# Kernel tuning notes

Measured on AMD Instinct MI355X. Metric: run time of the kernel, lower is better.

## Reference

```python
import jax, jax.numpy as jnp
import numpy as np

# dims
B, L, C = 2, 2048, 256          # batch, seq_len (== max_length), input_dim
H, D = 8, 32                     # num_head, head_dim
W = 3                            # avg-pool window along key axis


def setup_inputs() -> dict:
    key = jax.random.key(0)
    ks = jax.random.split(key, 7)
    g_qk = (2.0 / (C + H * D)) ** 0.5   # GlorotNormal std
    g_v = (2.0 / (C + H)) ** 0.5
    g_pe = (2.0 / (L + C)) ** 0.5
    return {
        "x":  jax.random.normal(ks[0], (B, L, C), dtype=jnp.float32),
        "Wq": jax.random.normal(ks[1], (C, H * D), dtype=jnp.float32) * g_qk,
        "bq": jnp.zeros((H, 1, 1, D), dtype=jnp.float32),
        "Wk": jax.random.normal(ks[2], (C, H * D), dtype=jnp.float32) * g_qk,
        "bk": jnp.zeros((H, 1, 1, D), dtype=jnp.float32),
        "Wv": jax.random.normal(ks[3], (C, H), dtype=jnp.float32) * g_v,
        "pe": jax.random.normal(ks[4], (L, C), dtype=jnp.float32) * g_pe,
    }


def reference(x, Wq, bq, Wk, bk, Wv, pe):
    b, l, _ = x.shape
    xq = x + pe                                   # (B,L,C) -- pe added to q and k inputs only
    q = (xq @ Wq).reshape(b, l, H, D).transpose(2, 0, 1, 3) + bq   # (H,B,L,D)
    k = (xq @ Wk).reshape(b, l, H, D).transpose(2, 0, 1, 3) + bk   # (H,B,L,D)
    v = (x @ Wv).transpose(2, 0, 1)               # (H,B,L) scalar gate per (head, pos)

    attn = jnp.einsum('hbqd,hbkd->hbqk', q, k) * (float(D) ** -0.5)  # (H,B,Lq,Lk)
    attn = jax.nn.softmax(attn, axis=-1)
    # band_part(-1, 0): keep lower triangle (q >= k), applied AFTER softmax
    causal = jnp.tril(jnp.ones((l, l), dtype=bool))
    attn = jnp.where(causal, attn, jnp.zeros((), attn.dtype))
    # scalar value gate along the query axis
    attn = attn * v[..., None]                    # (H,B,Lq,Lk)
    # avg-pool window W along key axis, SAME padding, pads excluded from count (TF semantics)
    sums = jax.lax.reduce_window(attn, 0.0, jax.lax.add, (1, 1, 1, W), (1, 1, 1, 1), 'SAME')
    counts = jax.lax.reduce_window(jnp.ones((l,), attn.dtype), 0.0, jax.lax.add, (W,), (1,), 'SAME')
    attn = sums / counts                          # broadcast (Lk,) over (H,B,Lq,Lk)
    # permute to (B,Lq,Lk,H) then global_mode sum over Lq  ->  (B,Lk,H)
    return jnp.sum(attn, axis=2).transpose(1, 2, 0)
```

## Files before the change

### kernel.cpp

```cpp
#include <hip/hip_runtime.h>

#define B 2
#define L 2048
#define C 256
#define H 8
#define D 32
#define HB 16
#define SCALE 0.17677669529663687f
#define LOG2E 1.4426950408889634f
#define QS (SCALE * LOG2E)

using bf16x8 = __attribute__((ext_vector_type(8))) __bf16;
using f32x4  = __attribute__((ext_vector_type(4))) float;

static __device__ inline unsigned short f2bf(float f) {
    unsigned u = __float_as_uint(f);
    return (unsigned short)((u + 0x7fffu + ((u >> 16) & 1u)) >> 16);
}
static __device__ inline unsigned pk2(float lo, float hi) {
    return (unsigned)f2bf(lo) | ((unsigned)f2bf(hi) << 16);
}

static __device__ inline float fexp2(float x) {
#if __has_builtin(__builtin_amdgcn_exp2f)
    return __builtin_amdgcn_exp2f(x);
#else
    float r; asm("v_exp_f32 %0, %1" : "=v"(r) : "v"(x)); return r;
#endif
}

__global__ __launch_bounds__(256) void prep_kernel(
    const float* __restrict__ x,
    const float* __restrict__ Wq,
    const float* __restrict__ Wk,
    const float* __restrict__ Wv,
    unsigned short* __restrict__ WqT,
    unsigned short* __restrict__ WkT,
    float* __restrict__ Vo)
{
    __shared__ float smem[64 * 65];
    const int t = threadIdx.x;

    if (blockIdx.x < 512) {
        float (*xrT)[8] = (float(*)[8])smem;
        float* vred = smem + 256 * 8;
        const int row0 = blockIdx.x * 8;
        const int b = row0 >> 11;
#pragma unroll
        for (int i = 0; i < 8; ++i)
            xrT[t][i] = x[(row0 + i) * C + t];
        __syncthreads();
        {
            const int cc = t >> 6, sub = t & 63, vi = sub >> 3, vh = sub & 7;
            float va = 0.f;
            for (int c = cc * 64; c < cc * 64 + 64; ++c)
                va += xrT[c][vi] * Wv[c * H + vh];
            vred[(cc * 8 + vi) * 8 + vh] = va;
        }
        __syncthreads();
        if (t < 64) {
            const int i2 = t >> 3, h2 = t & 7;
            const float v = vred[(0 * 8 + i2) * 8 + h2] + vred[(1 * 8 + i2) * 8 + h2] +
                            vred[(2 * 8 + i2) * 8 + h2] + vred[(3 * 8 + i2) * 8 + h2];
            const int l = (row0 + i2) & (L - 1);
            Vo[(h2 * B + b) * L + l] = v;
        }
    } else {
        const int bb = blockIdx.x - 512;
        const int mat = bb >> 4;
        const int tile = bb & 15, ci = tile >> 2, ni = tile & 3;
        const float* W = mat ? Wk : Wq;
        unsigned short* WT = mat ? WkT : WqT;
        const float s = mat ? 1.0f : QS;
        const int c0 = ci * 64, n0 = ni * 64;
        float (*ld)[65] = (float(*)[65])smem;
        const int tr = t >> 4, tc = (t & 15) * 4;
#pragma unroll
        for (int p = 0; p < 4; ++p) {
            const int lc = p * 16 + tr;
            const float4 v = *(const float4*)&W[(c0 + lc) * (H * D) + n0 + tc];
            ld[lc][tc] = v.x; ld[lc][tc + 1] = v.y;
            ld[lc][tc + 2] = v.z; ld[lc][tc + 3] = v.w;
        }
        __syncthreads();
#pragma unroll
        for (int p = 0; p < 4; ++p) {
            const int nl = p * 16 + tr;
            const unsigned lo = pk2(ld[tc][nl] * s, ld[tc + 1][nl] * s);
            const unsigned hi = pk2(ld[tc + 2][nl] * s, ld[tc + 3][nl] * s);
            uint2 u; u.x = lo; u.y = hi;
            *(uint2*)&WT[(n0 + nl) * C + c0 + tc] = u;
        }
    }
}

__global__ __launch_bounds__(256) void qk_gemm_kernel(
    const float* __restrict__ x, const float* __restrict__ pe,
    const unsigned short* __restrict__ WqT, const unsigned short* __restrict__ WkT,
    const float* __restrict__ bq, const float* __restrict__ bk,
    unsigned short* __restrict__ Qo, unsigned short* __restrict__ Ko)
{
    __shared__ uint4 xqs[16][32];
    const int t = threadIdx.x;
    const int w = t >> 6, lane = t & 63;
    const int quad = lane >> 4, col = lane & 15;
    const int row0 = (blockIdx.x >> 2) * 16;
    const int n0 = (blockIdx.x & 3) * 64;

    {
        const int srow = t >> 4, sc = (t & 15) * 16;
        const int grow = row0 + srow;
        const int gl = grow & (L - 1);
        const float* xp = x + (size_t)grow * C + sc;
        const float* pp = pe + (size_t)gl * C + sc;
        const float4 a0 = ((const float4*)xp)[0], a1 = ((const float4*)xp)[1];
        const float4 a2 = ((const float4*)xp)[2], a3 = ((const float4*)xp)[3];
        const float4 p0 = ((const float4*)pp)[0], p1 = ((const float4*)pp)[1];
        const float4 p2 = ((const float4*)pp)[2], p3 = ((const float4*)pp)[3];
        uint4 u0, u1;
        u0.x = pk2(a0.x + p0.x, a0.y + p0.y);
        u0.y = pk2(a0.z + p0.z, a0.w + p0.w);
        u0.z = pk2(a1.x + p1.x, a1.y + p1.y);
        u0.w = pk2(a1.z + p1.z, a1.w + p1.w);
        u1.x = pk2(a2.x + p2.x, a2.y + p2.y);
        u1.y = pk2(a2.z + p2.z, a2.w + p2.w);
        u1.z = pk2(a3.x + p3.x, a3.y + p3.y);
        u1.w = pk2(a3.z + p3.z, a3.w + p3.w);
        const int cb = (t & 15) * 2;
        xqs[srow][(cb + 0) ^ (srow & 7)] = u0;
        xqs[srow][(cb + 1) ^ (srow & 7)] = u1;
    }
    __syncthreads();

    bf16x8 af[8];
#pragma unroll
    for (int kk = 0; kk < 8; ++kk)
        af[kk] = *(const bf16x8*)&xqs[col][(kk * 4 + quad) ^ (col & 7)];

    const int n = n0 + w * 16 + col;
    const unsigned short* wq = WqT + (size_t)n * C;
    const unsigned short* wk = WkT + (size_t)n * C;
    f32x4 accq = {0.f, 0.f, 0.f, 0.f};
    f32x4 acck = {0.f, 0.f, 0.f, 0.f};
#pragma unroll
    for (int kk = 0; kk < 8; ++kk) {
        const bf16x8 bq8 = *(const bf16x8*)(wq + kk * 32 + quad * 8);
        const bf16x8 bk8 = *(const bf16x8*)(wk + kk * 32 + quad * 8);
        accq = __builtin_amdgcn_mfma_f32_16x16x32_bf16(af[kk], bq8, accq, 0, 0, 0);
        acck = __builtin_amdgcn_mfma_f32_16x16x32_bf16(af[kk], bk8, acck, 0, 0, 0);
    }

    const int h = n >> 5, d = n & 31;
    const float bqv = bq[n] * QS;
    const float bkv = bk[n];
#pragma unroll
    for (int r = 0; r < 4; ++r) {
        const int m = quad * 4 + r;
        const int grow = row0 + m, b = grow >> 11, l = grow & (L - 1);
        const size_t o = ((size_t)(h * B + b) * L + l) * D + d;
        Qo[o] = f2bf(accq[r] + bqv);
        Ko[o] = f2bf(acck[r] + bkv);
    }
}

__global__ __launch_bounds__(256) void passA_kernel(
    const __bf16* __restrict__ Qb, const __bf16* __restrict__ Kb,
    const float* __restrict__ V, float* __restrict__ G)
{
    __shared__ float lredA[4][4][4][16];
    __shared__ float lredB[4][4][4][16];
    const int tid = threadIdx.x;
    const int w = tid >> 6, lane = tid & 63;
    const int quad = lane >> 4, col = lane & 15;
    const int xcd = blockIdx.x & 7, g = blockIdx.x >> 3;
    const int hb = xcd * 2 + (g >> 6), p = g & 63;
    const __bf16* Qp = Qb + (size_t)hb * L * D;
    const __bf16* Kp = Kb + (size_t)hb * L * D;

    const bf16x8 qfa = *(const bf16x8*)(Qp + ((2 * p) * 16 + col) * D + quad * 8);
    const bf16x8 qfb = *(const bf16x8*)(Qp + ((2 * p + 1) * 16 + col) * D + quad * 8);
    const f32x4 zero = {0.f, 0.f, 0.f, 0.f};

    float la0 = 0.f, la1 = 0.f, la2 = 0.f, la3 = 0.f;
    float lb0 = 0.f, lb1 = 0.f, lb2 = 0.f, lb3 = 0.f;
    const __bf16* kp = Kp + (w * 512 + col) * D + quad * 8;
#pragma unroll 4
    for (int kt = 0; kt < 32; ++kt) {
        const bf16x8 kf = *(const bf16x8*)kp;
        kp += 16 * D;
        f32x4 a = __builtin_amdgcn_mfma_f32_16x16x32_bf16(qfa, kf, zero, 0, 0, 0);
        f32x4 bb = __builtin_amdgcn_mfma_f32_16x16x32_bf16(qfb, kf, zero, 0, 0, 0);
        la0 += fexp2(a[0]);  lb0 += fexp2(bb[0]);
        la1 += fexp2(a[1]);  lb1 += fexp2(bb[1]);
        la2 += fexp2(a[2]);  lb2 += fexp2(bb[2]);
        la3 += fexp2(a[3]);  lb3 += fexp2(bb[3]);
    }
    lredA[w][quad][0][col] = la0;  lredB[w][quad][0][col] = lb0;
    lredA[w][quad][1][col] = la1;  lredB[w][quad][1][col] = lb1;
    lredA[w][quad][2][col] = la2;  lredB[w][quad][2][col] = lb2;
    lredA[w][quad][3][col] = la3;  lredB[w][quad][3][col] = lb3;
    __syncthreads();
    if (tid < 32) {
        const int r8 = tid & 15;
        const int qd = r8 >> 2, r = r8 & 3;
        const float* base = (tid < 16) ? &lredA[0][0][0][0] : &lredB[0][0][0][0];
        float s = 0.f;
#pragma unroll
        for (int w2 = 0; w2 < 4; ++w2) {
            const float* pp = base + ((w2 * 4 + qd) * 4 + r) * 16;
#pragma unroll
            for (int c2 = 0; c2 < 16; ++c2) s += pp[c2];
        }
        const int qt = 2 * p + (tid >> 4);
        const int qq = hb * L + qt * 16 + r8;
        G[qq] = V[qq] / s;
    }
}

__global__ __launch_bounds__(256) void passB_kernel(
    const __bf16* __restrict__ Qb, const __bf16* __restrict__ Kb,
    const float* __restrict__ G, float* __restrict__ S)
{
    __shared__ float sred[2][4][4][16];
    const int tid = threadIdx.x;
    const int w = tid >> 6, lane = tid & 63;
    const int quad = lane >> 4, col = lane & 15;
    const int xcd = blockIdx.x & 7, g = blockIdx.x >> 3;
    const int hb = xcd * 2 + (g >> 6), p = g & 63;
    const int kb0 = 2 * p, kb1 = 2 * p + 1;
    const __bf16* Qp = Qb + (size_t)hb * L * D;
    const __bf16* Kp = Kb + (size_t)hb * L * D;
    const float* Gp = G + hb * L;

    const bf16x8 kf0 = *(const bf16x8*)(Kp + (kb0 * 16 + col) * D + quad * 8);
    const bf16x8 kf1 = *(const bf16x8*)(Kp + (kb1 * 16 + col) * D + quad * 8);
    const f32x4 zero = {0.f, 0.f, 0.f, 0.f};
    const int kidx0 = kb0 * 16 + col;
    const int kidx1 = kb1 * 16 + col;

    float s0 = 0.f, s1 = 0.f;
    int qt = kb0 + w;
    if (qt < 128) {
        const bf16x8 qf = *(const bf16x8*)(Qp + (qt * 16 + col) * D + quad * 8);
        const float4 gg = *(const float4*)(Gp + qt * 16 + quad * 4);
        const int qbase = qt * 16 + quad * 4;
        f32x4 a0 = __builtin_amdgcn_mfma_f32_16x16x32_bf16(qf, kf0, zero, 0, 0, 0);
        if (w == 0) {
            s0 += (qbase + 0 >= kidx0) ? fexp2(a0[0]) * gg.x : 0.f;
            s0 += (qbase + 1 >= kidx0) ? fexp2(a0[1]) * gg.y : 0.f;
            s0 += (qbase + 2 >= kidx0) ? fexp2(a0[2]) * gg.z : 0.f;
            s0 += (qbase + 3 >= kidx0) ? fexp2(a0[3]) * gg.w : 0.f;
        } else {
            s0 += fexp2(a0[0]) * gg.x + fexp2(a0[1]) * gg.y +
                  fexp2(a0[2]) * gg.z + fexp2(a0[3]) * gg.w;
            f32x4 a1 = __builtin_amdgcn_mfma_f32_16x16x32_bf16(qf, kf1, zero, 0, 0, 0);
            if (w == 1) {
                s1 += (qbase + 0 >= kidx1) ? fexp2(a1[0]) * gg.x : 0.f;
                s1 += (qbase + 1 >= kidx1) ? fexp2(a1[1]) * gg.y : 0.f;
                s1 += (qbase + 2 >= kidx1) ? fexp2(a1[2]) * gg.z : 0.f;
                s1 += (qbase + 3 >= kidx1) ? fexp2(a1[3]) * gg.w : 0.f;
            } else {
                s1 += fexp2(a1[0]) * gg.x + fexp2(a1[1]) * gg.y +
                      fexp2(a1[2]) * gg.z + fexp2(a1[3]) * gg.w;
            }
        }
        qt += 4;
    }
    for (; qt < 128; qt += 4) {
        const bf16x8 qf = *(const bf16x8*)(Qp + (qt * 16 + col) * D + quad * 8);
        const float4 gg = *(const float4*)(Gp + qt * 16 + quad * 4);
        f32x4 a0 = __builtin_amdgcn_mfma_f32_16x16x32_bf16(qf, kf0, zero, 0, 0, 0);
        f32x4 a1 = __builtin_amdgcn_mfma_f32_16x16x32_bf16(qf, kf1, zero, 0, 0, 0);
        s0 += fexp2(a0[0]) * gg.x + fexp2(a0[1]) * gg.y +
              fexp2(a0[2]) * gg.z + fexp2(a0[3]) * gg.w;
        s1 += fexp2(a1[0]) * gg.x + fexp2(a1[1]) * gg.y +
              fexp2(a1[2]) * gg.z + fexp2(a1[3]) * gg.w;
    }
    sred[0][w][quad][col] = s0;
    sred[1][w][quad][col] = s1;
    __syncthreads();
    if (tid < 32) {
        const int c = tid & 15, which = tid >> 4;
        float s = 0.f;
#pragma unroll
        for (int j = 0; j < 16; ++j) s += sred[which][j >> 2][j & 3][c];
        S[hb * L + (2 * p + which) * 16 + c] = s;
    }
}

__global__ __launch_bounds__(256) void pool_kernel(
    const float* __restrict__ S, float* __restrict__ out)
{
    const int flat = blockIdx.x * 256 + threadIdx.x;
    const int h = flat & 7;
    const int k = (flat >> 3) & (L - 1);
    const int b = flat >> 14;
    const float* Sb = S + (h * B + b) * L;
    float s = Sb[k];
    float cnt = 1.f;
    if (k > 0)     { s += Sb[k - 1]; cnt += 1.f; }
    if (k < L - 1) { s += Sb[k + 1]; cnt += 1.f; }
    out[flat] = s / cnt;
}

extern "C" void kernel_launch(void* const* d_in, const int* in_sizes, int n_in,
                              void* d_out, int out_size, void* d_ws, size_t ws_size,
                              hipStream_t stream)
{
    const float* x  = (const float*)d_in[0];
    const float* Wq = (const float*)d_in[1];
    const float* bq = (const float*)d_in[2];
    const float* Wk = (const float*)d_in[3];
    const float* bk = (const float*)d_in[4];
    const float* Wv = (const float*)d_in[5];
    const float* pe = (const float*)d_in[6];
    float* out = (float*)d_out;

    unsigned short* Qbf = (unsigned short*)d_ws;
    unsigned short* Kbf = Qbf + (size_t)HB * L * D;
    float* Vo = (float*)(Kbf + (size_t)HB * L * D);
    float* G  = Vo + (size_t)HB * L;
    float* S  = G  + (size_t)HB * L;
    unsigned short* WqT = (unsigned short*)(S + (size_t)HB * L);
    unsigned short* WkT = WqT + (size_t)C * H * D;

    prep_kernel<<<544, 256, 0, stream>>>(x, Wq, Wk, Wv, WqT, WkT, Vo);
    qk_gemm_kernel<<<1024, 256, 0, stream>>>(x, pe, WqT, WkT, bq, bk, Qbf, Kbf);
    passA_kernel<<<1024, 256, 0, stream>>>(
        (const __bf16*)Qbf, (const __bf16*)Kbf, Vo, G);
    passB_kernel<<<1024, 256, 0, stream>>>(
        (const __bf16*)Qbf, (const __bf16*)Kbf, G, S);
    pool_kernel<<<(B * L * H) / 256, 256, 0, stream>>>(S, out);
}
```

Before: 107.2 us.

## Fuse V projection into QK GEMM, pool into passB, pre-swizzle weights

Splits the prep kernel: weight transposition now writes weights directly in MFMA fragment order so GEMM B-loads become contiguous, while the x@Wv projection is folded into the QK GEMM blocks of quarter 0. The pool kernel is removed and replaced by a last-block-done atomic counter in passB that performs the window average per head-batch. Cross-lane reductions in passA/passB switch from shared-memory sums to wave shuffles, and launch bounds add occupancy hints. This saves kernel launches and memory traffic, but adds atomic/fence overhead and puts extra work on a quarter of the GEMM blocks.

```diff
diff --git a/kernel.cpp b/kernel.cpp
--- a/kernel.cpp
+++ b/kernel.cpp
@@ -29,86 +29,57 @@
 #endif
 }
 
-__global__ __launch_bounds__(256) void prep_kernel(
-    const float* __restrict__ x,
+__global__ __launch_bounds__(256) void wtrans_kernel(
     const float* __restrict__ Wq,
     const float* __restrict__ Wk,
-    const float* __restrict__ Wv,
     unsigned short* __restrict__ WqT,
     unsigned short* __restrict__ WkT,
-    float* __restrict__ Vo)
-{
-    __shared__ float smem[64 * 65];
+    unsigned int* __restrict__ cnt)
+{
     const int t = threadIdx.x;
-
-    if (blockIdx.x < 512) {
-        float (*xrT)[8] = (float(*)[8])smem;
-        float* vred = smem + 256 * 8;
-        const int row0 = blockIdx.x * 8;
-        const int b = row0 >> 11;
-#pragma unroll
-        for (int i = 0; i < 8; ++i)
-            xrT[t][i] = x[(row0 + i) * C + t];
-        __syncthreads();
-        {
-            const int cc = t >> 6, sub = t & 63, vi = sub >> 3, vh = sub & 7;
-            float va = 0.f;
-            for (int c = cc * 64; c < cc * 64 + 64; ++c)
-                va += xrT[c][vi] * Wv[c * H + vh];
-            vred[(cc * 8 + vi) * 8 + vh] = va;
-        }
-        __syncthreads();
-        if (t < 64) {
-            const int i2 = t >> 3, h2 = t & 7;
-            const float v = vred[(0 * 8 + i2) * 8 + h2] + vred[(1 * 8 + i2) * 8 + h2] +
-                            vred[(2 * 8 + i2) * 8 + h2] + vred[(3 * 8 + i2) * 8 + h2];
-            const int l = (row0 + i2) & (L - 1);
-            Vo[(h2 * B + b) * L + l] = v;
-        }
-    } else {
-        const int bb = blockIdx.x - 512;
-        const int mat = bb >> 4;
-        const int tile = bb & 15, ci = tile >> 2, ni = tile & 3;
-        const float* W = mat ? Wk : Wq;
-        unsigned short* WT = mat ? WkT : WqT;
-        const float s = mat ? 1.0f : QS;
-        const int c0 = ci * 64, n0 = ni * 64;
-        float (*ld)[65] = (float(*)[65])smem;
-        const int tr = t >> 4, tc = (t & 15) * 4;
-#pragma unroll
-        for (int p = 0; p < 4; ++p) {
-            const int lc = p * 16 + tr;
-            const float4 v = *(const float4*)&W[(c0 + lc) * (H * D) + n0 + tc];
-            ld[lc][tc] = v.x; ld[lc][tc + 1] = v.y;
-            ld[lc][tc + 2] = v.z; ld[lc][tc + 3] = v.w;
-        }
-        __syncthreads();
-#pragma unroll
-        for (int p = 0; p < 4; ++p) {
-            const int nl = p * 16 + tr;
-            const unsigned lo = pk2(ld[tc][nl] * s, ld[tc + 1][nl] * s);
-            const unsigned hi = pk2(ld[tc + 2][nl] * s, ld[tc + 3][nl] * s);
-            uint2 u; u.x = lo; u.y = hi;
-            *(uint2*)&WT[(n0 + nl) * C + c0 + tc] = u;
-        }
-    }
-}
-
-__global__ __launch_bounds__(256) void qk_gemm_kernel(
+    if (blockIdx.x == 0 && t < HB) cnt[t] = 0;
+
+    const int mat = blockIdx.x >> 5;
+    const int fid = (blockIdx.x & 31) * 256 + t;
+    const int col = fid & 15;
+    const int quad = (fid >> 4) & 3;
+    const int kk = (fid >> 6) & 7;
+    const int nt = fid >> 9;
+    const int n = nt * 16 + col;
+    const int c0 = kk * 32 + quad * 8;
+    const float* W = mat ? Wk : Wq;
+    unsigned short* WT = mat ? WkT : WqT;
+    const float s = mat ? 1.0f : QS;
+
+    float v[8];
+#pragma unroll
+    for (int j = 0; j < 8; ++j)
+        v[j] = W[(c0 + j) * (H * D) + n] * s;
+    uint4 u;
+    u.x = pk2(v[0], v[1]); u.y = pk2(v[2], v[3]);
+    u.z = pk2(v[4], v[5]); u.w = pk2(v[6], v[7]);
+    *(uint4*)(WT + (size_t)fid * 8) = u;
+}
+
+__global__ __launch_bounds__(256, 4) void qk_gemm_kernel(
     const float* __restrict__ x, const float* __restrict__ pe,
     const unsigned short* __restrict__ WqT, const unsigned short* __restrict__ WkT,
     const float* __restrict__ bq, const float* __restrict__ bk,
-    unsigned short* __restrict__ Qo, unsigned short* __restrict__ Ko)
+    const float* __restrict__ Wv,
+    unsigned short* __restrict__ Qo, unsigned short* __restrict__ Ko,
+    float* __restrict__ Vo)
 {
     __shared__ uint4 xqs[16][32];
+    __shared__ float vpart[16][16][9];
     const int t = threadIdx.x;
     const int w = t >> 6, lane = t & 63;
     const int quad = lane >> 4, col = lane & 15;
     const int row0 = (blockIdx.x >> 2) * 16;
-    const int n0 = (blockIdx.x & 3) * 64;
+    const int quarter = blockIdx.x & 3;
+    const int doV = (quarter == 0);
 
     {
-        const int srow = t >> 4, sc = (t & 15) * 16;
+        const int srow = t >> 4, scIdx = t & 15, sc = scIdx * 16;
         const int grow = row0 + srow;
         const int gl = grow & (L - 1);
         const float* xp = x + (size_t)grow * C + sc;
@@ -126,30 +97,60 @@
         u1.y = pk2(a2.z + p2.z, a2.w + p2.w);
         u1.z = pk2(a3.x + p3.x, a3.y + p3.y);
         u1.w = pk2(a3.z + p3.z, a3.w + p3.w);
-        const int cb = (t & 15) * 2;
+        const int cb = scIdx * 2;
         xqs[srow][(cb + 0) ^ (srow & 7)] = u0;
         xqs[srow][(cb + 1) ^ (srow & 7)] = u1;
-    }
-    __syncthreads();
+
+        if (doV) {
+            float vp[8];
+#pragma unroll
+            for (int hh = 0; hh < 8; ++hh) vp[hh] = 0.f;
+            const float xs[16] = {a0.x, a0.y, a0.z, a0.w, a1.x, a1.y, a1.z, a1.w,
+                                  a2.x, a2.y, a2.z, a2.w, a3.x, a3.y, a3.z, a3.w};
+#pragma unroll
+            for (int j = 0; j < 16; ++j) {
+                const float4 wv0 = *(const float4*)&Wv[(sc + j) * H];
+                const float4 wv1 = *(const float4*)&Wv[(sc + j) * H + 4];
+                vp[0] += xs[j] * wv0.x; vp[1] += xs[j] * wv0.y;
+                vp[2] += xs[j] * wv0.z; vp[3] += xs[j] * wv0.w;
+                vp[4] += xs[j] * wv1.x; vp[5] += xs[j] * wv1.y;
+                vp[6] += xs[j] * wv1.z; vp[7] += xs[j] * wv1.w;
+            }
+#pragma unroll
+            for (int hh = 0; hh < 8; ++hh) vpart[srow][scIdx][hh] = vp[hh];
+        }
+    }
+    __syncthreads();
+
+    if (doV && t < 128) {
+        const int srow2 = t >> 3, h2 = t & 7;
+        float v = 0.f;
+#pragma unroll
+        for (int i = 0; i < 16; ++i) v += vpart[srow2][i][h2];
+        const int grow = row0 + srow2, b = grow >> 11, l = grow & (L - 1);
+        Vo[(h2 * B + b) * L + l] = v;
+    }
 
     bf16x8 af[8];
 #pragma unroll
     for (int kk = 0; kk < 8; ++kk)
         af[kk] = *(const bf16x8*)&xqs[col][(kk * 4 + quad) ^ (col & 7)];
 
-    const int n = n0 + w * 16 + col;
-    const unsigned short* wq = WqT + (size_t)n * C;
-    const unsigned short* wk = WkT + (size_t)n * C;
+    const int nt = quarter * 4 + w;
+    const unsigned short* wq = WqT + ((size_t)nt * 8 * 4 * 16) * 8;
+    const unsigned short* wk = WkT + ((size_t)nt * 8 * 4 * 16) * 8;
+    const int foff = (quad * 16 + col) * 8;
     f32x4 accq = {0.f, 0.f, 0.f, 0.f};
     f32x4 acck = {0.f, 0.f, 0.f, 0.f};
 #pragma unroll
     for (int kk = 0; kk < 8; ++kk) {
-        const bf16x8 bq8 = *(const bf16x8*)(wq + kk * 32 + quad * 8);
-        const bf16x8 bk8 = *(const bf16x8*)(wk + kk * 32 + quad * 8);
+        const bf16x8 bq8 = *(const bf16x8*)(wq + kk * 512 + foff);
+        const bf16x8 bk8 = *(const bf16x8*)(wk + kk * 512 + foff);
         accq = __builtin_amdgcn_mfma_f32_16x16x32_bf16(af[kk], bq8, accq, 0, 0, 0);
         acck = __builtin_amdgcn_mfma_f32_16x16x32_bf16(af[kk], bk8, acck, 0, 0, 0);
     }
 
+    const int n = nt * 16 + col;
     const int h = n >> 5, d = n & 31;
     const float bqv = bq[n] * QS;
     const float bkv = bk[n];
@@ -163,12 +164,11 @@
     }
 }
 
-__global__ __launch_bounds__(256) void passA_kernel(
+__global__ __launch_bounds__(256, 4) void passA_kernel(
     const __bf16* __restrict__ Qb, const __bf16* __restrict__ Kb,
     const float* __restrict__ V, float* __restrict__ G)
 {
-    __shared__ float lredA[4][4][4][16];
-    __shared__ float lredB[4][4][4][16];
+    __shared__ float lred2[4][4][8];
     const int tid = threadIdx.x;
     const int w = tid >> 6, lane = tid & 63;
     const int quad = lane >> 4, col = lane & 15;
@@ -181,8 +181,9 @@
     const bf16x8 qfb = *(const bf16x8*)(Qp + ((2 * p + 1) * 16 + col) * D + quad * 8);
     const f32x4 zero = {0.f, 0.f, 0.f, 0.f};
 
-    float la0 = 0.f, la1 = 0.f, la2 = 0.f, la3 = 0.f;
-    float lb0 = 0.f, lb1 = 0.f, lb2 = 0.f, lb3 = 0.f;
+    float acc[8];
+#pragma unroll
+    for (int i = 0; i < 8; ++i) acc[i] = 0.f;
     const __bf16* kp = Kp + (w * 512 + col) * D + quad * 8;
 #pragma unroll 4
     for (int kt = 0; kt < 32; ++kt) {
@@ -190,38 +191,42 @@
         kp += 16 * D;
         f32x4 a = __builtin_amdgcn_mfma_f32_16x16x32_bf16(qfa, kf, zero, 0, 0, 0);
         f32x4 bb = __builtin_amdgcn_mfma_f32_16x16x32_bf16(qfb, kf, zero, 0, 0, 0);
-        la0 += fexp2(a[0]);  lb0 += fexp2(bb[0]);
-        la1 += fexp2(a[1]);  lb1 += fexp2(bb[1]);
-        la2 += fexp2(a[2]);  lb2 += fexp2(bb[2]);
-        la3 += fexp2(a[3]);  lb3 += fexp2(bb[3]);
-    }
-    lredA[w][quad][0][col] = la0;  lredB[w][quad][0][col] = lb0;
-    lredA[w][quad][1][col] = la1;  lredB[w][quad][1][col] = lb1;
-    lredA[w][quad][2][col] = la2;  lredB[w][quad][2][col] = lb2;
-    lredA[w][quad][3][col] = la3;  lredB[w][quad][3][col] = lb3;
+        acc[0] += fexp2(a[0]);  acc[4] += fexp2(bb[0]);
+        acc[1] += fexp2(a[1]);  acc[5] += fexp2(bb[1]);
+        acc[2] += fexp2(a[2]);  acc[6] += fexp2(bb[2]);
+        acc[3] += fexp2(a[3]);  acc[7] += fexp2(bb[3]);
+    }
+#pragma unroll
+    for (int i = 0; i < 8; ++i) {
+        float v = acc[i];
+        v += __shfl_xor(v, 1);
+        v += __shfl_xor(v, 2);
+        v += __shfl_xor(v, 4);
+        v += __shfl_xor(v, 8);
+        acc[i] = v;
+    }
+    if (col == 0) {
+#pragma unroll
+        for (int i = 0; i < 8; ++i) lred2[w][quad][i] = acc[i];
+    }
     __syncthreads();
     if (tid < 32) {
-        const int r8 = tid & 15;
-        const int qd = r8 >> 2, r = r8 & 3;
-        const float* base = (tid < 16) ? &lredA[0][0][0][0] : &lredB[0][0][0][0];
-        float s = 0.f;
-#pragma unroll
-        for (int w2 = 0; w2 < 4; ++w2) {
-            const float* pp = base + ((w2 * 4 + qd) * 4 + r) * 16;
-#pragma unroll
-            for (int c2 = 0; c2 < 16; ++c2) s += pp[c2];
-        }
-        const int qt = 2 * p + (tid >> 4);
-        const int qq = hb * L + qt * 16 + r8;
+        const int tile = tid >> 4, idx = tid & 15;
+        const int qd = idx >> 2, r = idx & 3;
+        const float s = lred2[0][qd][tile * 4 + r] + lred2[1][qd][tile * 4 + r] +
+                        lred2[2][qd][tile * 4 + r] + lred2[3][qd][tile * 4 + r];
+        const int qq = hb * L + (2 * p + tile) * 16 + idx;
         G[qq] = V[qq] / s;
     }
 }
 
-__global__ __launch_bounds__(256) void passB_kernel(
+__global__ __launch_bounds__(256, 4) void passB_kernel(
     const __bf16* __restrict__ Qb, const __bf16* __restrict__ Kb,
-    const float* __restrict__ G, float* __restrict__ S)
-{
-    __shared__ float sred[2][4][4][16];
+    const float* __restrict__ G, float* __restrict__ S,
+    unsigned int* __restrict__ cnt, float* __restrict__ out)
+{
+    __shared__ float sred[4][2][16];
+    __shared__ int lastf;
     const int tid = threadIdx.x;
     const int w = tid >> 6, lane = tid & 63;
     const int quad = lane >> 4, col = lane & 15;
@@ -266,6 +271,7 @@
         }
         qt += 4;
     }
+#pragma unroll 2
     for (; qt < 128; qt += 4) {
         const bf16x8 qf = *(const bf16x8*)(Qp + (qt * 16 + col) * D + quad * 8);
         const float4 gg = *(const float4*)(Gp + qt * 16 + quad * 4);
@@ -276,31 +282,37 @@
         s1 += fexp2(a1[0]) * gg.x + fexp2(a1[1]) * gg.y +
               fexp2(a1[2]) * gg.z + fexp2(a1[3]) * gg.w;
     }
-    sred[0][w][quad][col] = s0;
-    sred[1][w][quad][col] = s1;
+    s0 += __shfl_xor(s0, 16); s0 += __shfl_xor(s0, 32);
+    s1 += __shfl_xor(s1, 16); s1 += __shfl_xor(s1, 32);
+    if (lane < 16) { sred[w][0][lane] = s0; sred[w][1][lane] = s1; }
     __syncthreads();
     if (tid < 32) {
-        const int c = tid & 15, which = tid >> 4;
-        float s = 0.f;
-#pragma unroll
-        for (int j = 0; j < 16; ++j) s += sred[which][j >> 2][j & 3][c];
+        const int which = tid >> 4, c = tid & 15;
+        const float s = sred[0][which][c] + sred[1][which][c] +
+                        sred[2][which][c] + sred[3][which][c];
         S[hb * L + (2 * p + which) * 16 + c] = s;
     }
-}
-
-__global__ __launch_bounds__(256) void pool_kernel(
-    const float* __restrict__ S, float* __restrict__ out)
-{
-    const int flat = blockIdx.x * 256 + threadIdx.x;
-    const int h = flat & 7;
-    const int k = (flat >> 3) & (L - 1);
-    const int b = flat >> 14;
-    const float* Sb = S + (h * B + b) * L;
-    float s = Sb[k];
-    float cnt = 1.f;
-    if (k > 0)     { s += Sb[k - 1]; cnt += 1.f; }
-    if (k < L - 1) { s += Sb[k + 1]; cnt += 1.f; }
-    out[flat] = s / cnt;
+    __syncthreads();
+    if (tid == 0) {
+        __threadfence();
+        const unsigned old = atomicAdd(&cnt[hb], 1u);
+        lastf = (old == 63u);
+    }
+    __syncthreads();
+    if (lastf) {
+        __threadfence();
+        const int h = hb >> 1, b = hb & 1;
+        const float* Sb = S + (size_t)hb * L;
+#pragma unroll
+        for (int i = 0; i < 8; ++i) {
+            const int k = i * 256 + tid;
+            float s = Sb[k];
+            float n = 1.f;
+            if (k > 0)     { s += Sb[k - 1]; n += 1.f; }
+            if (k < L - 1) { s += Sb[k + 1]; n += 1.f; }
+            out[((size_t)b * L + k) * H + h] = s / n;
+        }
+    }
 }
 
 extern "C" void kernel_launch(void* const* d_in, const int* in_sizes, int n_in,
@@ -323,12 +335,13 @@
     float* S  = G  + (size_t)HB * L;
     unsigned short* WqT = (unsigned short*)(S + (size_t)HB * L);
     unsigned short* WkT = WqT + (size_t)C * H * D;
-
-    prep_kernel<<<544, 256, 0, stream>>>(x, Wq, Wk, Wv, WqT, WkT, Vo);
-    qk_gemm_kernel<<<1024, 256, 0, stream>>>(x, pe, WqT, WkT, bq, bk, Qbf, Kbf);
+    unsigned int* cnt = (unsigned int*)(WkT + (size_t)C * H * D);
+
+    wtrans_kernel<<<64, 256, 0, stream>>>(Wq, Wk, WqT, WkT, cnt);
+    qk_gemm_kernel<<<1024, 256, 0, stream>>>(x, pe, WqT, WkT, bq, bk, Wv,
+                                             Qbf, Kbf, Vo);
     passA_kernel<<<1024, 256, 0, stream>>>(
         (const __bf16*)Qbf, (const __bf16*)Kbf, Vo, G);
     passB_kernel<<<1024, 256, 0, stream>>>(
-        (const __bf16*)Qbf, (const __bf16*)Kbf, G, S);
-    pool_kernel<<<(B * L * H) / 256, 256, 0, stream>>>(S, out);
-}
+        (const __bf16*)Qbf, (const __bf16*)Kbf, G, S, cnt, out);
+}
```

After: 130.5 us. 21.8% more time.
